# Kernel tuning notes

Measured on AMD Instinct MI355X. Metric: run time of the kernel, lower is better.

## Reference

```python
import jax, jax.numpy as jnp
import numpy as np


def setup_inputs() -> dict:
    key = jax.random.key(0)
    k1, k2, k3, k4 = jax.random.split(key, 4)
    B, H, S, E, L = 2, 12, 256, 64, 25
    return {
        "attention_probs": jax.random.uniform(k1, (B, H, S, S), dtype=jnp.float32),
        "value_attentions": jax.random.normal(k2, (B, H, S, E), dtype=jnp.float32),
        "relative_positions": jax.random.normal(k3, (B, S, S, H * E), dtype=jnp.float32),
        "W": jax.random.normal(k4, (L, H * E), dtype=jnp.float32) * 0.02,
        "b": jnp.zeros((L,), dtype=jnp.float32),
    }


def reference(attention_probs, value_attentions, relative_positions, W, b):
    # Faithful translation of TransformerMHSLayer.forward:
    #   out[b,h,i,j,e] = p[b,h,i,j] * (v[b,h,j,e] + rel[b,i,j,h,e])
    #   pre[b,j,i,l]   = sum_{h,e} out[b,h,i,j,e] * W[l, h*E+e] + bias[l]
    #   logits[b,j,l,i] = pre[b,j,i,l]
    B, H, S, E = value_attentions.shape
    L = W.shape[0]
    Wr = W.reshape(L, H, E)                       # [L,H,E], matches h*E+e flattening
    rel = relative_positions.reshape(B, S, S, H, E)  # view(B,S,S,H,E)
    # value term: contract v with W per head, then weight by attention probs
    pre = jnp.einsum('bhij,bhje,lhe->bjil', attention_probs, value_attentions, Wr)
    # relative-position term (same attention weighting)
    pre = pre + jnp.einsum('bhij,bijhe,lhe->bjil', attention_probs, rel, Wr)
    pre = pre + b                                  # bias over label dim
    return pre.transpose(0, 1, 3, 2)               # [B, S(j), L, S(i)]
```

## Files before the change

### kernel.cpp

```cpp
#include <hip/hip_runtime.h>
#include <stdint.h>


#define Bb 2
#define Hh 12
#define Ss 256
#define Ee 64
#define Ll 25
#define Kk 768

typedef __attribute__((ext_vector_type(8))) short bf16x8;
typedef __attribute__((ext_vector_type(4))) float f32x4;

#define NFRAG (Hh * 4)
#define AB_BYTES ((size_t)NFRAG * 64 * 8 * 2)
#define PT_BYTES ((size_t)Bb * Ss * Hh * Ss * 4)

__device__ __forceinline__ ushort f2bf(float x) {
    union { float f; uint32_t u; } u; u.f = x;
    uint32_t r = u.u + 0x7fff + ((u.u >> 16) & 1);
    return (ushort)(r >> 16);
}

__global__ void a_pack_kernel(const float* __restrict__ W, ushort* __restrict__ ab) {
    int idx = blockIdx.x * 256 + threadIdx.x;
    if (idx >= NFRAG * 64) return;
    int lane = idx & 63, fi = idx >> 6;
    int Lt = fi & 1, ks = (fi >> 1) & 1, h = fi >> 2;
    int l = Lt * 16 + (lane & 15);
    int k0 = h * Ee + ks * 32 + (lane >> 4) * 8;
    ushort* dst = ab + (size_t)idx * 8;
#pragma unroll
    for (int t = 0; t < 8; ++t)
        dst[t] = (l < Ll) ? f2bf(W[l * Kk + k0 + t]) : (ushort)0;
}

__global__ void p_transpose_kernel(const float* __restrict__ p,
                                   float* __restrict__ pt) {
    __shared__ float tile[32][33];
    const int bh = blockIdx.y;
    const int b = bh / Hh, h = bh % Hh;
    const int ti = blockIdx.x >> 3, tj = blockIdx.x & 7;
    const int tx = threadIdx.x & 31, ty = threadIdx.x >> 5;
#pragma unroll
    for (int s = 0; s < 4; ++s) {
        const int il = ty + 8 * s;
        tile[il][tx] = p[((size_t)(b * Hh + h) * Ss + ti * 32 + il) * Ss + tj * 32 + tx];
    }
    __syncthreads();
#pragma unroll
    for (int s = 0; s < 4; ++s) {
        const int jl = ty + 8 * s;
        pt[((size_t)(b * Ss + tj * 32 + jl) * Hh + h) * Ss + ti * 32 + tx] = tile[tx][jl];
    }
}

template <bool FULL>
__global__ __launch_bounds__(256, 4) void mhs_mfma(
    const float* __restrict__ p,
    const float* __restrict__ pt,
    const float* __restrict__ v,
    const float* __restrict__ rel,
    const float* __restrict__ W,
    const ushort* __restrict__ ab,
    const float* __restrict__ bias,
    float* __restrict__ out)
{
    const int g = blockIdx.x;
    const int ig = g & 3, j = (g >> 2) & (Ss - 1), b = g >> 10;
    const int tid = threadIdx.x;
    const int w = tid >> 6, lane = tid & 63;
    const int col = lane & 15, grp = lane >> 4;
    const int iw = ig * 64 + w * 16 + col;

    const float* relp = rel + ((size_t)(b * Ss + iw) * Ss + j) * Kk + grp * 8;

    f32x4 acc0 = {0.f, 0.f, 0.f, 0.f};
    f32x4 acc1 = {0.f, 0.f, 0.f, 0.f};

    float4 c0 = *(const float4*)(relp);
    float4 c1 = *(const float4*)(relp + 4);
    float4 c2 = *(const float4*)(relp + 32);
    float4 c3 = *(const float4*)(relp + 36);

#pragma unroll 1
    for (int h = 0; h < Hh; ++h) {
        const int hn = (h + 1 < Hh) ? h + 1 : h;
        const float* rn = relp + hn * Ee;
        const float4 n0 = *(const float4*)(rn);
        const float4 n1 = *(const float4*)(rn + 4);
        const float4 n2 = *(const float4*)(rn + 32);
        const float4 n3 = *(const float4*)(rn + 36);

        bf16x8 A00, A01, A10, A11;
        if (FULL) {
            const ushort* abase = ab + (size_t)(h * 4) * 512 + lane * 8;
            A00 = *(const bf16x8*)(abase);
            A01 = *(const bf16x8*)(abase + 512);
            A10 = *(const bf16x8*)(abase + 1024);
            A11 = *(const bf16x8*)(abase + 1536);
        } else {
#pragma unroll
            for (int t = 0; t < 8; ++t) {
                const int kb = h * Ee + grp * 8 + t;
                const int la = col, lb = 16 + col;
                A00[t] = (short)f2bf(W[la * Kk + kb]);
                A01[t] = (lb < Ll) ? (short)f2bf(W[lb * Kk + kb]) : (short)0;
                A10[t] = (short)f2bf(W[la * Kk + kb + 32]);
                A11[t] = (lb < Ll) ? (short)f2bf(W[lb * Kk + kb + 32]) : (short)0;
            }
        }

        const float* vbp = v + ((size_t)(b * Hh + h) * Ss + j) * Ee + grp * 8;
        const float4 va0 = *(const float4*)(vbp);
        const float4 va1 = *(const float4*)(vbp + 4);
        const float4 vc0 = *(const float4*)(vbp + 32);
        const float4 vc1 = *(const float4*)(vbp + 36);

        const float pv = FULL
            ? pt[((size_t)(b * Ss + j) * Hh + h) * Ss + iw]
            : p[((size_t)(b * Hh + h) * Ss + iw) * Ss + j];

        bf16x8 B0, B1;
#pragma unroll
        for (int t = 0; t < 4; ++t) {
            B0[t]     = (short)f2bf(((const float*)&c0)[t] + ((const float*)&va0)[t]);
            B0[t + 4] = (short)f2bf(((const float*)&c1)[t] + ((const float*)&va1)[t]);
            B1[t]     = (short)f2bf(((const float*)&c2)[t] + ((const float*)&vc0)[t]);
            B1[t + 4] = (short)f2bf(((const float*)&c3)[t] + ((const float*)&vc1)[t]);
        }
        f32x4 C0 = {0.f, 0.f, 0.f, 0.f}, C1 = {0.f, 0.f, 0.f, 0.f};
        C0 = __builtin_amdgcn_mfma_f32_16x16x32_bf16(A00, B0, C0, 0, 0, 0);
        C0 = __builtin_amdgcn_mfma_f32_16x16x32_bf16(A10, B1, C0, 0, 0, 0);
        C1 = __builtin_amdgcn_mfma_f32_16x16x32_bf16(A01, B0, C1, 0, 0, 0);
        C1 = __builtin_amdgcn_mfma_f32_16x16x32_bf16(A11, B1, C1, 0, 0, 0);
        acc0 += pv * C0;
        acc1 += pv * C1;

        c0 = n0; c1 = n1; c2 = n2; c3 = n3;
    }

#pragma unroll
    for (int r = 0; r < 4; ++r) {
        const int l0 = grp * 4 + r;
        out[((size_t)(b * Ss + j) * Ll + l0) * Ss + iw] = acc0[r] + bias[l0];
        const int l1 = 16 + grp * 4 + r;
        if (l1 < Ll)
            out[((size_t)(b * Ss + j) * Ll + l1) * Ss + iw] = acc1[r] + bias[l1];
    }
}

extern "C" void kernel_launch(void* const* d_in, const int* in_sizes, int n_in,
                              void* d_out, int out_size, void* d_ws, size_t ws_size,
                              hipStream_t stream) {
    const float* p    = (const float*)d_in[0];
    const float* v    = (const float*)d_in[1];
    const float* rel  = (const float*)d_in[2];
    const float* W    = (const float*)d_in[3];
    const float* bias = (const float*)d_in[4];
    float* out = (float*)d_out;

    const int nblk = Bb * Ss * 4;
    const bool full = ws_size >= AB_BYTES + PT_BYTES;

    if (full) {
        ushort* ab = (ushort*)d_ws;
        float* pt = (float*)((char*)d_ws + AB_BYTES);
        hipLaunchKernelGGL(a_pack_kernel, dim3((NFRAG * 64 + 255) / 256), dim3(256),
                           0, stream, W, ab);
        hipLaunchKernelGGL(p_transpose_kernel, dim3(64, Bb * Hh), dim3(256),
                           0, stream, p, pt);
        hipLaunchKernelGGL((mhs_mfma<true>), dim3(nblk), dim3(256), 0, stream,
                           p, pt, v, rel, W, ab, bias, out);
    } else {
        hipLaunchKernelGGL((mhs_mfma<false>), dim3(nblk), dim3(256), 0, stream,
                           p, (const float*)nullptr, v, rel, W,
                           (const ushort*)nullptr, bias, out);
    }
}
```

Before: 112.4 us.

## Precompute W·v per head and double-buffer rel/A operand loads

The value term is split out algebraically: a new small kernel computes W·v for each (b,j,h,l) in fp32. The main kernel then adds it to the MFMA result instead of adding v to rel before the bf16 conversion, which removes the per-iteration v loads. The head loop is restructured with two operand sets, so loads for the next head are issued while the current head's MFMAs run. This adds a kernel launch, extra workspace traffic and register pressure, and it requires a larger workspace for the fast path to be taken.

```diff
diff --git a/kernel.cpp b/kernel.cpp
--- a/kernel.cpp
+++ b/kernel.cpp
@@ -15,6 +15,7 @@
 #define NFRAG (Hh * 4)
 #define AB_BYTES ((size_t)NFRAG * 64 * 8 * 2)
 #define PT_BYTES ((size_t)Bb * Ss * Hh * Ss * 4)
+#define WV_BYTES ((size_t)Bb * Ss * Hh * 32 * 4)
 
 __device__ __forceinline__ ushort f2bf(float x) {
     union { float f; uint32_t u; } u; u.f = x;
@@ -55,14 +56,34 @@
     }
 }
 
-template <bool FULL>
-__global__ __launch_bounds__(256, 4) void mhs_mfma(
-    const float* __restrict__ p,
+__global__ void wv_kernel(const float* __restrict__ W, const float* __restrict__ v,
+                          float* __restrict__ wv) {
+    const int bj = blockIdx.x;
+    const int b = bj >> 8, j = bj & (Ss - 1);
+    const int t = threadIdx.x;
+    const int h = t >> 5, l = t & 31;
+    float acc = 0.f;
+    if (l < Ll) {
+        const float* wrow = W + l * Kk + h * Ee;
+        const float* vrow = v + ((size_t)(b * Hh + h) * Ss + j) * Ee;
+#pragma unroll
+        for (int e = 0; e < Ee; ++e) acc = __builtin_fmaf(wrow[e], vrow[e], acc);
+    }
+    wv[((size_t)bj * Hh + h) * 32 + l] = acc;
+}
+
+struct Ops {
+    float4 c0, c1, c2, c3;
+    bf16x8 A00, A01, A10, A11;
+    float4 w0, w1;
+    float pv;
+};
+
+__global__ __launch_bounds__(256, 4) void mhs_pipe(
     const float* __restrict__ pt,
-    const float* __restrict__ v,
     const float* __restrict__ rel,
-    const float* __restrict__ W,
     const ushort* __restrict__ ab,
+    const float* __restrict__ wv,
     const float* __restrict__ bias,
     float* __restrict__ out)
 {
@@ -74,53 +95,107 @@
     const int iw = ig * 64 + w * 16 + col;
 
     const float* relp = rel + ((size_t)(b * Ss + iw) * Ss + j) * Kk + grp * 8;
+    const ushort* abl = ab + lane * 8;
+    const float* wvb = wv + ((size_t)(b * Ss + j) * Hh) * 32 + grp * 4;
+    const float* ptb = pt + ((size_t)(b * Ss + j) * Hh) * Ss + iw;
 
     f32x4 acc0 = {0.f, 0.f, 0.f, 0.f};
     f32x4 acc1 = {0.f, 0.f, 0.f, 0.f};
 
-    float4 c0 = *(const float4*)(relp);
-    float4 c1 = *(const float4*)(relp + 4);
-    float4 c2 = *(const float4*)(relp + 32);
-    float4 c3 = *(const float4*)(relp + 36);
-
+    auto load_ops = [&](Ops& o, int h) {
+        const float* rb = relp + h * Ee;
+        o.c0 = *(const float4*)(rb);
+        o.c1 = *(const float4*)(rb + 4);
+        o.c2 = *(const float4*)(rb + 32);
+        o.c3 = *(const float4*)(rb + 36);
+        const ushort* ap = abl + (size_t)h * 2048;
+        o.A00 = *(const bf16x8*)(ap);
+        o.A01 = *(const bf16x8*)(ap + 512);
+        o.A10 = *(const bf16x8*)(ap + 1024);
+        o.A11 = *(const bf16x8*)(ap + 1536);
+        const float* wp = wvb + h * 32;
+        o.w0 = *(const float4*)(wp);
+        o.w1 = *(const float4*)(wp + 16);
+        o.pv = ptb[h * Ss];
+    };
+
+    auto compute = [&](const Ops& o) {
+        bf16x8 B0, B1;
+#pragma unroll
+        for (int t = 0; t < 4; ++t) {
+            B0[t]     = (short)f2bf(((const float*)&o.c0)[t]);
+            B0[t + 4] = (short)f2bf(((const float*)&o.c1)[t]);
+            B1[t]     = (short)f2bf(((const float*)&o.c2)[t]);
+            B1[t + 4] = (short)f2bf(((const float*)&o.c3)[t]);
+        }
+        f32x4 C0 = {0.f, 0.f, 0.f, 0.f}, C1 = {0.f, 0.f, 0.f, 0.f};
+        C0 = __builtin_amdgcn_mfma_f32_16x16x32_bf16(o.A00, B0, C0, 0, 0, 0);
+        C0 = __builtin_amdgcn_mfma_f32_16x16x32_bf16(o.A10, B1, C0, 0, 0, 0);
+        C1 = __builtin_amdgcn_mfma_f32_16x16x32_bf16(o.A01, B0, C1, 0, 0, 0);
+        C1 = __builtin_amdgcn_mfma_f32_16x16x32_bf16(o.A11, B1, C1, 0, 0, 0);
+        const f32x4 wv0 = {o.w0.x, o.w0.y, o.w0.z, o.w0.w};
+        const f32x4 wv1 = {o.w1.x, o.w1.y, o.w1.z, o.w1.w};
+        acc0 += o.pv * (C0 + wv0);
+        acc1 += o.pv * (C1 + wv1);
+    };
+
+    Ops oa, ob;
+    load_ops(oa, 0);
+#pragma unroll 1
+    for (int h = 0; h < Hh; h += 2) {
+        load_ops(ob, h + 1);
+        compute(oa);
+        load_ops(oa, (h + 2 < Hh) ? h + 2 : Hh - 1);
+        compute(ob);
+    }
+
+#pragma unroll
+    for (int r = 0; r < 4; ++r) {
+        const int l0 = grp * 4 + r;
+        out[((size_t)(b * Ss + j) * Ll + l0) * Ss + iw] = acc0[r] + bias[l0];
+        const int l1 = 16 + grp * 4 + r;
+        if (l1 < Ll)
+            out[((size_t)(b * Ss + j) * Ll + l1) * Ss + iw] = acc1[r] + bias[l1];
+    }
+}
+
+__global__ __launch_bounds__(256, 4) void mhs_basic(
+    const float* __restrict__ p, const float* __restrict__ v,
+    const float* __restrict__ rel, const float* __restrict__ W,
+    const float* __restrict__ bias, float* __restrict__ out)
+{
+    const int g = blockIdx.x;
+    const int ig = g & 3, j = (g >> 2) & (Ss - 1), b = g >> 10;
+    const int tid = threadIdx.x;
+    const int w = tid >> 6, lane = tid & 63;
+    const int col = lane & 15, grp = lane >> 4;
+    const int iw = ig * 64 + w * 16 + col;
+    const float* relp = rel + ((size_t)(b * Ss + iw) * Ss + j) * Kk + grp * 8;
+
+    f32x4 acc0 = {0.f, 0.f, 0.f, 0.f}, acc1 = {0.f, 0.f, 0.f, 0.f};
 #pragma unroll 1
     for (int h = 0; h < Hh; ++h) {
-        const int hn = (h + 1 < Hh) ? h + 1 : h;
-        const float* rn = relp + hn * Ee;
-        const float4 n0 = *(const float4*)(rn);
-        const float4 n1 = *(const float4*)(rn + 4);
-        const float4 n2 = *(const float4*)(rn + 32);
-        const float4 n3 = *(const float4*)(rn + 36);
-
         bf16x8 A00, A01, A10, A11;
-        if (FULL) {
-            const ushort* abase = ab + (size_t)(h * 4) * 512 + lane * 8;
-            A00 = *(const bf16x8*)(abase);
-            A01 = *(const bf16x8*)(abase + 512);
-            A10 = *(const bf16x8*)(abase + 1024);
-            A11 = *(const bf16x8*)(abase + 1536);
-        } else {
-#pragma unroll
-            for (int t = 0; t < 8; ++t) {
-                const int kb = h * Ee + grp * 8 + t;
-                const int la = col, lb = 16 + col;
-                A00[t] = (short)f2bf(W[la * Kk + kb]);
-                A01[t] = (lb < Ll) ? (short)f2bf(W[lb * Kk + kb]) : (short)0;
-                A10[t] = (short)f2bf(W[la * Kk + kb + 32]);
-                A11[t] = (lb < Ll) ? (short)f2bf(W[lb * Kk + kb + 32]) : (short)0;
-            }
+#pragma unroll
+        for (int t = 0; t < 8; ++t) {
+            const int kb = h * Ee + grp * 8 + t;
+            const int la = col, lb = 16 + col;
+            A00[t] = (short)f2bf(W[la * Kk + kb]);
+            A01[t] = (lb < Ll) ? (short)f2bf(W[lb * Kk + kb]) : (short)0;
+            A10[t] = (short)f2bf(W[la * Kk + kb + 32]);
+            A11[t] = (lb < Ll) ? (short)f2bf(W[lb * Kk + kb + 32]) : (short)0;
         }
-
         const float* vbp = v + ((size_t)(b * Hh + h) * Ss + j) * Ee + grp * 8;
         const float4 va0 = *(const float4*)(vbp);
         const float4 va1 = *(const float4*)(vbp + 4);
         const float4 vc0 = *(const float4*)(vbp + 32);
         const float4 vc1 = *(const float4*)(vbp + 36);
-
-        const float pv = FULL
-            ? pt[((size_t)(b * Ss + j) * Hh + h) * Ss + iw]
-            : p[((size_t)(b * Hh + h) * Ss + iw) * Ss + j];
-
+        const float* rb = relp + h * Ee;
+        const float4 c0 = *(const float4*)(rb);
+        const float4 c1 = *(const float4*)(rb + 4);
+        const float4 c2 = *(const float4*)(rb + 32);
+        const float4 c3 = *(const float4*)(rb + 36);
+        const float pv = p[((size_t)(b * Hh + h) * Ss + iw) * Ss + j];
         bf16x8 B0, B1;
 #pragma unroll
         for (int t = 0; t < 4; ++t) {
@@ -136,10 +211,7 @@
         C1 = __builtin_amdgcn_mfma_f32_16x16x32_bf16(A11, B1, C1, 0, 0, 0);
         acc0 += pv * C0;
         acc1 += pv * C1;
-
-        c0 = n0; c1 = n1; c2 = n2; c3 = n3;
-    }
-
+    }
 #pragma unroll
     for (int r = 0; r < 4; ++r) {
         const int l0 = grp * 4 + r;
@@ -161,20 +233,22 @@
     float* out = (float*)d_out;
 
     const int nblk = Bb * Ss * 4;
-    const bool full = ws_size >= AB_BYTES + PT_BYTES;
+    const bool full = ws_size >= AB_BYTES + PT_BYTES + WV_BYTES;
 
     if (full) {
         ushort* ab = (ushort*)d_ws;
         float* pt = (float*)((char*)d_ws + AB_BYTES);
+        float* wvp = (float*)((char*)d_ws + AB_BYTES + PT_BYTES);
         hipLaunchKernelGGL(a_pack_kernel, dim3((NFRAG * 64 + 255) / 256), dim3(256),
                            0, stream, W, ab);
         hipLaunchKernelGGL(p_transpose_kernel, dim3(64, Bb * Hh), dim3(256),
                            0, stream, p, pt);
-        hipLaunchKernelGGL((mhs_mfma<true>), dim3(nblk), dim3(256), 0, stream,
-                           p, pt, v, rel, W, ab, bias, out);
+        hipLaunchKernelGGL(wv_kernel, dim3(Bb * Ss), dim3(Hh * 32),
+                           0, stream, W, v, wvp);
+        hipLaunchKernelGGL(mhs_pipe, dim3(nblk), dim3(256), 0, stream,
+                           pt, rel, ab, wvp, bias, out);
     } else {
-        hipLaunchKernelGGL((mhs_mfma<false>), dim3(nblk), dim3(256), 0, stream,
-                           p, (const float*)nullptr, v, rel, W,
-                           (const ushort*)nullptr, bias, out);
-    }
-}
+        hipLaunchKernelGGL(mhs_basic, dim3(nblk), dim3(256), 0, stream,
+                           p, v, rel, W, bias, out);
+    }
+}
```

Result: slower. 124.5 us (+10.7%).
